# Optimization experiments

Hardware: AMD Instinct MI355X
Metric: run time of the kernel (lower is better)

The kernel has to match this reference:

```python
import jax
jax.config.update("jax_enable_x64", True)
import jax.numpy as jnp
import numpy as np

# NTT-friendly stand-in prime for BLS12-377 Fr (residues fit in int64, products in 62 bits)
P = 2013265921          # 15 * 2^27 + 1
GEN = 31                # generator of (Z/P)^*
COSET = 7               # coset shift generator
LOG_DOMAIN = 21
DOMAIN = 1 << LOG_DOMAIN
BATCH = 8


def _pow_table(base, length):
    """numpy int64 table [base^0, ..., base^(length-1)] mod P, built by doubling."""
    t = np.ones(length, dtype=np.int64)
    k = 1
    while k < length:
        mult = pow(int(base), k, P)          # exact python-int exponentiation
        end = min(2 * k, length)
        t[k:end] = (t[:end - k] * mult) % P  # < 2^62, no overflow
        k = end
    return t


def _bitrev(n):
    b = int(n).bit_length() - 1
    idx = np.arange(n, dtype=np.int64)
    rev = np.zeros(n, dtype=np.int64)
    for i in range(b):
        rev |= ((idx >> i) & 1) << (b - 1 - i)
    return rev


def _ntt_core(x, inverse):
    """Iterative radix-2 Cooley-Tukey NTT over rows of x: [batch, n] int64 residues mod P."""
    b, n = x.shape
    logn = n.bit_length() - 1
    root = pow(GEN, (P - 1) // n, P)         # primitive n-th root of unity
    if inverse:
        root = pow(root, P - 2, P)
    wpow = _pow_table(root, n // 2)          # root^j, j < n/2 (host-side, exact)
    x = x[:, jnp.asarray(_bitrev(n))]        # bit-reversal permutation
    for s in range(1, logn + 1):             # structural loop over log2(n) stages
        m = 1 << s
        half = m >> 1
        tw = jnp.asarray(wpow[:: n // m][:half])   # stage twiddles root^{j*n/m}
        xr = x.reshape(b, n // m, m)
        e, o = xr[..., :half], xr[..., half:]
        t = (o * tw) % P                     # butterfly: vectorized over all groups
        x = jnp.concatenate([(e + t) % P, (e - t) % P], axis=-1).reshape(b, n)
    return x


def setup_inputs() -> dict:
    key = jax.random.key(0)
    inp = jax.random.randint(key, (BATCH, DOMAIN), 0, P, dtype=jnp.int64)
    return {"input": inp, "is_intt": 0, "is_coset": 0}


def reference(input, is_intt, is_coset):
    x = jnp.mod(input, P)
    n = x.shape[-1]
    if (not is_intt) and is_coset:
        # coset NTT: multiply element i by COSET^i before the forward transform
        x = (x * jnp.asarray(_pow_table(COSET, n))) % P
    x = _ntt_core(x, inverse=bool(is_intt))
    if is_intt:
        if is_coset:
            # coset INTT: undo the coset shift after the inverse transform
            x = (x * jnp.asarray(_pow_table(pow(COSET, P - 2, P), n))) % P
        n_inv = pow(int(n), P - 2, P)
        x = (x * n_inv) % P                  # scale by n^{-1}
    return x
```

## Files before the change

### kernel.cpp

```cpp
#include <hip/hip_runtime.h>
#include <stdint.h>

typedef unsigned int u32;
typedef unsigned long long u64;

#define MOD_P 2013265921u

#define T_A      0
#define T_B      16384
#define T_W128P  32768
#define T_RP     49152
#define T_CLP    49216
#define T_CHP    65600
#define T_NINV   65728

__device__ __forceinline__ u32 mul64mod(u32 a, u32 b){ return (u32)((u64)a * b % MOD_P); }

__device__ u32 powmod(u32 b, u32 e){
  u32 r = 1;
  while (e){ if (e & 1) r = mul64mod(r, b); b = mul64mod(b, b); e >>= 1; }
  return r;
}

__device__ __forceinline__ u32 shoup_of(u32 v){ return (u32)(((u64)v << 32) / MOD_P); }

__device__ __forceinline__ u32 redP(u32 a){
  u32 b = a - MOD_P;
  return b < a ? b : a;
}

__device__ __forceinline__ u32 mul_shoup(u32 a, uint2 t){
  u32 q = __umulhi(a, t.y);
  u32 r = a * t.x - q * MOD_P;
  return redP(r);
}

__device__ __forceinline__ constexpr int rev4(int m){
  return ((m&1)<<3) | ((m&2)<<1) | ((m&4)>>1) | ((m&8)>>3);
}

__device__ __forceinline__ void bf(u32 &x, u32 &y, uint2 t){
  u32 s = redP(x + y);
  u32 d = redP(x - y + MOD_P);
  x = s; y = mul_shoup(d, t);
}
__device__ __forceinline__ void bf0(u32 &x, u32 &y){
  u32 s = redP(x + y);
  u32 d = redP(x - y + MOD_P);
  x = s; y = d;
}

__device__ __forceinline__ void stages_p1(u32 v[16], int b, const uint2* __restrict__ twl){
  #pragma unroll
  for (int m = 0; m < 8; ++m) bf(v[m], v[m+8], twl[b + 8*m]);
  #pragma unroll
  for (int g = 0; g < 2; ++g)
    #pragma unroll
    for (int m = 0; m < 4; ++m) bf(v[g*8+m], v[g*8+m+4], twl[(b + 8*m) << 1]);
  #pragma unroll
  for (int g = 0; g < 4; ++g)
    #pragma unroll
    for (int m = 0; m < 2; ++m) bf(v[g*4+m], v[g*4+m+2], twl[(b + 8*m) << 2]);
  #pragma unroll
  for (int k = 0; k < 8; ++k) bf(v[2*k], v[2*k+1], twl[b << 3]);
}
__device__ __forceinline__ void stages_p2(u32 v[16], const uint2* __restrict__ twl){
  #pragma unroll
  for (int g = 0; g < 2; ++g)
    #pragma unroll
    for (int m = 0; m < 4; ++m) bf(v[g*8+m], v[g*8+m+4], twl[m << 4]);
  #pragma unroll
  for (int g = 0; g < 4; ++g)
    #pragma unroll
    for (int m = 0; m < 2; ++m) bf(v[g*4+m], v[g*4+m+2], twl[m << 5]);
  #pragma unroll
  for (int k = 0; k < 8; ++k) bf0(v[2*k], v[2*k+1]);
}

extern "C" __global__ void k_gen(uint2* __restrict__ tw, const int* __restrict__ f_intt){
  const int idx = blockIdx.x * 256 + threadIdx.x;
  const int intt = f_intt[0];
  u32 w = powmod(31u, (MOD_P - 1) >> 21);
  if (intt) w = powmod(w, MOD_P - 2);
  const u32 w128 = powmod(w, 128u);
  const int hi = idx >> 7, lo = idx & 127;

  u32 a = powmod(w, (u32)(hi * lo));
  tw[T_A + idx] = make_uint2(a, shoup_of(a));
  u32 b = powmod(w128, (u32)(hi * lo));
  tw[T_B + idx] = make_uint2(b, shoup_of(b));
  u32 v2 = powmod(w128, (u32)idx);
  tw[T_W128P + idx] = make_uint2(v2, shoup_of(v2));
  u32 c = intt ? powmod(7u, MOD_P - 2) : 7u;
  u32 cv = powmod(c, (u32)idx);
  tw[T_CLP + idx] = make_uint2(cv, shoup_of(cv));
  if (idx < 128){
    u32 h = powmod(c, (u32)idx << 14);
    tw[T_CHP + idx] = make_uint2(h, shoup_of(h));
  }
  if (idx < 64){
    u32 rv = powmod(powmod(w, 1u << 14), (u32)idx);
    tw[T_RP + idx] = make_uint2(rv, shoup_of(rv));
  }
  if (idx == 0){
    u32 ninv = powmod(1u << 21, MOD_P - 2);
    tw[T_NINV] = make_uint2(ninv, shoup_of(ninv));
  }
}

extern "C" __global__ void __launch_bounds__(512, 8) k_passA(
    const u32* __restrict__ x, u32* __restrict__ y, const uint2* __restrict__ tw,
    const int* __restrict__ f_intt, const int* __restrict__ f_coset)
{
  __shared__ u32 lds[8192];
  const int wg = blockIdx.x;
  const int half = wg & 1;
  const int jb = (wg >> 1) & 127;
  const int batch = wg >> 8;
  const int t = threadIdx.x;
  const int c = t & 63;
  const int b = __builtin_amdgcn_readfirstlane(t >> 6);
  const int jc = (half << 6) | c;
  const u32* xb = x + ((size_t)batch << 21);
  u32* yb = y + ((size_t)batch << 21);
  const uint2* twl = tw + T_RP;

  u32 v[16];
  #pragma unroll
  for (int m = 0; m < 16; ++m){
    u32 a = xb[((size_t)(b + 8*m) << 14) + (jb << 7) + jc];
    v[m] = redP(a);
  }
  if ((f_intt[0] == 0) && (f_coset[0] != 0)){
    uint2 cl = tw[T_CLP + (jb << 7) + jc];
    #pragma unroll
    for (int m = 0; m < 16; ++m){
      v[m] = mul_shoup(v[m], cl);
      v[m] = mul_shoup(v[m], tw[T_CHP + b + 8*m]);
    }
  }
  stages_p1(v, b, twl);
  #pragma unroll
  for (int m = 0; m < 16; ++m) lds[((b + 8*m) << 6) | c] = v[m];
  __syncthreads();
  #pragma unroll
  for (int m = 0; m < 16; ++m) v[m] = lds[((16*b + m) << 6) | c];
  stages_p2(v, twl);
  const int rb = ((b&1)<<2) | (b&2) | ((b&4)>>2);
  #pragma unroll
  for (int m = 0; m < 16; ++m){
    const int ka = (rev4(m) << 3) | rb;
    u32 vv = mul_shoup(v[m], tw[T_A + (ka << 7) + jc]);
    vv = mul_shoup(vv, tw[T_W128P + ka * jb]);
    yb[((size_t)ka << 14) + (jb << 7) + jc] = vv;
  }
}

extern "C" __global__ void __launch_bounds__(512, 8) k_passB(
    u32* __restrict__ y, const uint2* __restrict__ tw)
{
  __shared__ u32 lds[8192];
  const int wg = blockIdx.x;
  const int half = wg & 1;
  const int ka = (wg >> 1) & 127;
  const int batch = wg >> 8;
  const int t = threadIdx.x;
  const int c = t & 63;
  const int b = __builtin_amdgcn_readfirstlane(t >> 6);
  const int jc = (half << 6) | c;
  u32* yb = y + ((size_t)batch << 21) + ((size_t)ka << 14);
  const uint2* twl = tw + T_RP;

  u32 v[16];
  #pragma unroll
  for (int m = 0; m < 16; ++m) v[m] = yb[((b + 8*m) << 7) + jc];
  stages_p1(v, b, twl);
  #pragma unroll
  for (int m = 0; m < 16; ++m) lds[((b + 8*m) << 6) | c] = v[m];
  __syncthreads();
  #pragma unroll
  for (int m = 0; m < 16; ++m) v[m] = lds[((16*b + m) << 6) | c];
  stages_p2(v, twl);
  const int rb = ((b&1)<<2) | (b&2) | ((b&4)>>2);
  #pragma unroll
  for (int m = 0; m < 16; ++m){
    const int kb = (rev4(m) << 3) | rb;
    u32 vv = mul_shoup(v[m], tw[T_B + (kb << 7) + jc]);
    yb[(kb << 7) + jc] = vv;
  }
}

__device__ __forceinline__ int cidx(int row, int a){
  return (row << 6) | (a ^ (row >> 2));
}
extern "C" __global__ void __launch_bounds__(512, 8) k_passC(
    u32* __restrict__ y, const uint2* __restrict__ tw,
    const int* __restrict__ f_intt, const int* __restrict__ f_coset)
{
  __shared__ u32 lds[8192];
  const int wg = blockIdx.x;
  const int half = wg & 1;
  const int kb = (wg >> 1) & 127;
  const int batch = wg >> 8;
  u32* yb = y + ((size_t)batch << 21);
  const u32* base = yb + (kb << 7);
  const int t = threadIdx.x;
  {
    const int q = t & 31;
    const int rr = t >> 5;
    #pragma unroll
    for (int i = 0; i < 4; ++i){
      int kaL = rr + 16*i;
      uint4 v4 = *(const uint4*)(base + ((size_t)((half << 6) + kaL) << 14) + (q << 2));
      lds[cidx(4*q+0, kaL)] = v4.x;
      lds[cidx(4*q+1, kaL)] = v4.y;
      lds[cidx(4*q+2, kaL)] = v4.z;
      lds[cidx(4*q+3, kaL)] = v4.w;
    }
  }
  __syncthreads();
  const int a = t & 63;
  const int b = __builtin_amdgcn_readfirstlane(t >> 6);
  const uint2* twl = tw + T_RP;
  u32 v[16];
  #pragma unroll
  for (int m = 0; m < 16; ++m) v[m] = lds[cidx(b + 8*m, a)];
  stages_p1(v, b, twl);
  #pragma unroll
  for (int m = 0; m < 16; ++m) lds[cidx(b + 8*m, a)] = v[m];
  __syncthreads();
  #pragma unroll
  for (int m = 0; m < 16; ++m) v[m] = lds[cidx(16*b + m, a)];
  stages_p2(v, twl);
  const int rb = ((b&1)<<2) | (b&2) | ((b&4)>>2);
  const int kaG = (half << 6) | a;
  const int intt = f_intt[0];
  const int coset = f_coset[0];
  #pragma unroll
  for (int m = 0; m < 16; ++m){
    const int kc = (rev4(m) << 3) | rb;
    u32 vv = v[m];
    if (intt){
      vv = mul_shoup(vv, tw[T_NINV]);
      if (coset){
        vv = mul_shoup(vv, tw[T_CLP + (kb << 7) + kaG]);
        vv = mul_shoup(vv, tw[T_CHP + kc]);
      }
    }
    yb[((size_t)kc << 14) + (kb << 7) + kaG] = vv;
  }
}

extern "C" void kernel_launch(void* const* d_in, const int* in_sizes, int n_in,
                              void* d_out, int out_size, void* d_ws, size_t ws_size,
                              hipStream_t stream)
{
  const u32* x = (const u32*)d_in[0];
  const int* f_intt  = (const int*)d_in[1];
  const int* f_coset = (const int*)d_in[2];
  u32* y   = (u32*)d_out;
  uint2* tw = (uint2*)d_ws;
  const int batch = in_sizes[0] >> 21;
  const int nwg = batch << 8;

  k_gen  <<<64,  256, 0, stream>>>(tw, f_intt);
  k_passA<<<nwg, 512, 0, stream>>>(x, y, tw, f_intt, f_coset);
  k_passB<<<nwg, 512, 0, stream>>>(y, tw);
  k_passC<<<nwg, 512, 0, stream>>>(y, tw, f_intt, f_coset);
}
```

Measured before the change: 103.8 us.

## Double NTT workgroups to 1024 threads over full 128-column tiles; lazy-reduce butterflies

Each of the three NTT passes now uses one 1024-thread workgroup per 128-column tile instead of two 512-thread halves. This halves the grid, gives wider contiguous global row accesses and doubles LDS per block to 64 KB. Separately, the butterfly difference is left unreduced in [0, 2P), because the following Shoup multiply tolerates it. A final reduction is added in pass C's forward path. The larger blocks and LDS footprint reduce how many workgroups fit per CU, and the launch-bounds hint may squeeze registers.

```diff
diff --git a/kernel.cpp b/kernel.cpp
--- a/kernel.cpp
+++ b/kernel.cpp
@@ -41,12 +41,12 @@
 
 __device__ __forceinline__ void bf(u32 &x, u32 &y, uint2 t){
   u32 s = redP(x + y);
-  u32 d = redP(x - y + MOD_P);
+  u32 d = x - y + MOD_P;
   x = s; y = mul_shoup(d, t);
 }
 __device__ __forceinline__ void bf0(u32 &x, u32 &y){
   u32 s = redP(x + y);
-  u32 d = redP(x - y + MOD_P);
+  u32 d = x - y + MOD_P;
   x = s; y = d;
 }
 
@@ -108,19 +108,17 @@
   }
 }
 
-extern "C" __global__ void __launch_bounds__(512, 8) k_passA(
+extern "C" __global__ void __launch_bounds__(1024, 8) k_passA(
     const u32* __restrict__ x, u32* __restrict__ y, const uint2* __restrict__ tw,
     const int* __restrict__ f_intt, const int* __restrict__ f_coset)
 {
-  __shared__ u32 lds[8192];
+  __shared__ u32 lds[16384];
   const int wg = blockIdx.x;
-  const int half = wg & 1;
-  const int jb = (wg >> 1) & 127;
-  const int batch = wg >> 8;
+  const int jb = wg & 127;
+  const int batch = wg >> 7;
   const int t = threadIdx.x;
-  const int c = t & 63;
-  const int b = __builtin_amdgcn_readfirstlane(t >> 6);
-  const int jc = (half << 6) | c;
+  const int jc = t & 127;
+  const int b = __builtin_amdgcn_readfirstlane(t >> 7);
   const u32* xb = x + ((size_t)batch << 21);
   u32* yb = y + ((size_t)batch << 21);
   const uint2* twl = tw + T_RP;
@@ -141,10 +139,10 @@
   }
   stages_p1(v, b, twl);
   #pragma unroll
-  for (int m = 0; m < 16; ++m) lds[((b + 8*m) << 6) | c] = v[m];
-  __syncthreads();
-  #pragma unroll
-  for (int m = 0; m < 16; ++m) v[m] = lds[((16*b + m) << 6) | c];
+  for (int m = 0; m < 16; ++m) lds[((b + 8*m) << 7) | jc] = v[m];
+  __syncthreads();
+  #pragma unroll
+  for (int m = 0; m < 16; ++m) v[m] = lds[((16*b + m) << 7) | jc];
   stages_p2(v, twl);
   const int rb = ((b&1)<<2) | (b&2) | ((b&4)>>2);
   #pragma unroll
@@ -156,18 +154,16 @@
   }
 }
 
-extern "C" __global__ void __launch_bounds__(512, 8) k_passB(
+extern "C" __global__ void __launch_bounds__(1024, 8) k_passB(
     u32* __restrict__ y, const uint2* __restrict__ tw)
 {
-  __shared__ u32 lds[8192];
+  __shared__ u32 lds[16384];
   const int wg = blockIdx.x;
-  const int half = wg & 1;
-  const int ka = (wg >> 1) & 127;
-  const int batch = wg >> 8;
+  const int ka = wg & 127;
+  const int batch = wg >> 7;
   const int t = threadIdx.x;
-  const int c = t & 63;
-  const int b = __builtin_amdgcn_readfirstlane(t >> 6);
-  const int jc = (half << 6) | c;
+  const int jc = t & 127;
+  const int b = __builtin_amdgcn_readfirstlane(t >> 7);
   u32* yb = y + ((size_t)batch << 21) + ((size_t)ka << 14);
   const uint2* twl = tw + T_RP;
 
@@ -176,10 +172,10 @@
   for (int m = 0; m < 16; ++m) v[m] = yb[((b + 8*m) << 7) + jc];
   stages_p1(v, b, twl);
   #pragma unroll
-  for (int m = 0; m < 16; ++m) lds[((b + 8*m) << 6) | c] = v[m];
-  __syncthreads();
-  #pragma unroll
-  for (int m = 0; m < 16; ++m) v[m] = lds[((16*b + m) << 6) | c];
+  for (int m = 0; m < 16; ++m) lds[((b + 8*m) << 7) | jc] = v[m];
+  __syncthreads();
+  #pragma unroll
+  for (int m = 0; m < 16; ++m) v[m] = lds[((16*b + m) << 7) | jc];
   stages_p2(v, twl);
   const int rb = ((b&1)<<2) | (b&2) | ((b&4)>>2);
   #pragma unroll
@@ -191,17 +187,16 @@
 }
 
 __device__ __forceinline__ int cidx(int row, int a){
-  return (row << 6) | (a ^ (row >> 2));
-}
-extern "C" __global__ void __launch_bounds__(512, 8) k_passC(
+  return (row << 7) | (a ^ (row >> 2));
+}
+extern "C" __global__ void __launch_bounds__(1024, 8) k_passC(
     u32* __restrict__ y, const uint2* __restrict__ tw,
     const int* __restrict__ f_intt, const int* __restrict__ f_coset)
 {
-  __shared__ u32 lds[8192];
+  __shared__ u32 lds[16384];
   const int wg = blockIdx.x;
-  const int half = wg & 1;
-  const int kb = (wg >> 1) & 127;
-  const int batch = wg >> 8;
+  const int kb = wg & 127;
+  const int batch = wg >> 7;
   u32* yb = y + ((size_t)batch << 21);
   const u32* base = yb + (kb << 7);
   const int t = threadIdx.x;
@@ -210,8 +205,8 @@
     const int rr = t >> 5;
     #pragma unroll
     for (int i = 0; i < 4; ++i){
-      int kaL = rr + 16*i;
-      uint4 v4 = *(const uint4*)(base + ((size_t)((half << 6) + kaL) << 14) + (q << 2));
+      int kaL = rr + 32*i;
+      uint4 v4 = *(const uint4*)(base + ((size_t)kaL << 14) + (q << 2));
       lds[cidx(4*q+0, kaL)] = v4.x;
       lds[cidx(4*q+1, kaL)] = v4.y;
       lds[cidx(4*q+2, kaL)] = v4.z;
@@ -219,8 +214,8 @@
     }
   }
   __syncthreads();
-  const int a = t & 63;
-  const int b = __builtin_amdgcn_readfirstlane(t >> 6);
+  const int a = t & 127;
+  const int b = __builtin_amdgcn_readfirstlane(t >> 7);
   const uint2* twl = tw + T_RP;
   u32 v[16];
   #pragma unroll
@@ -233,7 +228,6 @@
   for (int m = 0; m < 16; ++m) v[m] = lds[cidx(16*b + m, a)];
   stages_p2(v, twl);
   const int rb = ((b&1)<<2) | (b&2) | ((b&4)>>2);
-  const int kaG = (half << 6) | a;
   const int intt = f_intt[0];
   const int coset = f_coset[0];
   #pragma unroll
@@ -243,11 +237,13 @@
     if (intt){
       vv = mul_shoup(vv, tw[T_NINV]);
       if (coset){
-        vv = mul_shoup(vv, tw[T_CLP + (kb << 7) + kaG]);
+        vv = mul_shoup(vv, tw[T_CLP + (kb << 7) + a]);
         vv = mul_shoup(vv, tw[T_CHP + kc]);
       }
+    } else {
+      vv = redP(vv);
     }
-    yb[((size_t)kc << 14) + (kb << 7) + kaG] = vv;
+    yb[((size_t)kc << 14) + (kb << 7) + a] = vv;
   }
 }
 
@@ -261,10 +257,10 @@
   u32* y   = (u32*)d_out;
   uint2* tw = (uint2*)d_ws;
   const int batch = in_sizes[0] >> 21;
-  const int nwg = batch << 8;
-
-  k_gen  <<<64,  256, 0, stream>>>(tw, f_intt);
-  k_passA<<<nwg, 512, 0, stream>>>(x, y, tw, f_intt, f_coset);
-  k_passB<<<nwg, 512, 0, stream>>>(y, tw);
-  k_passC<<<nwg, 512, 0, stream>>>(y, tw, f_intt, f_coset);
-}
+  const int nwg = batch << 7;
+
+  k_gen  <<<64,   256, 0, stream>>>(tw, f_intt);
+  k_passA<<<nwg, 1024, 0, stream>>>(x, y, tw, f_intt, f_coset);
+  k_passB<<<nwg, 1024, 0, stream>>>(y, tw);
+  k_passC<<<nwg, 1024, 0, stream>>>(y, tw, f_intt, f_coset);
+}
```

Result: slower. 107.0 us (+3.0%).
